# Performance work log

Hardware: AMD Instinct MI355X
Metric: run time of the kernel (lower is better)

Reference implementation:

```python
import jax, jax.numpy as jnp
import numpy as np

B, T = 64, 2048
DQ, A, E = 1024, 128, 512
NF, K = 32, 31
PAD = (K - 1) // 2


def setup_inputs() -> dict:
    key = jax.random.key(0)
    ks = jax.random.split(key, 8)
    s = 0.02
    return {
        "query": jax.random.normal(ks[0], (B, 1, DQ), jnp.float32),
        "memory": jax.random.normal(ks[1], (B, T, E), jnp.float32),
        "attention_weights_cat": jax.random.uniform(ks[2], (B, 2, T), jnp.float32),
        "W_query": jax.random.normal(ks[3], (A, DQ), jnp.float32) * s,
        "W_memory": jax.random.normal(ks[4], (A, E), jnp.float32) * s,
        "conv_w": jax.random.normal(ks[5], (NF, 2, K), jnp.float32) * s,
        "W_loc": jax.random.normal(ks[6], (A, NF), jnp.float32) * s,
        "v": jax.random.normal(ks[7], (1, A), jnp.float32) * s,
    }


def reference(query, memory, attention_weights_cat, W_query, W_memory, conv_w, W_loc, v):
    # projected key: [B, T, A]
    key = jnp.einsum("bte,ae->bta", memory, W_memory)
    # projected query: [B, 1, A]
    q = jnp.einsum("bsd,ad->bsa", query, W_query)
    # location features: Conv1d (2 -> NF, same padding, no bias) then linear to A
    loc = jax.lax.conv_general_dilated(
        attention_weights_cat, conv_w,
        window_strides=(1,), padding=[(PAD, PAD)],
        dimension_numbers=("NCH", "OIH", "NCH"))  # [B, NF, T]
    loc = jnp.einsum("bft,af->bta", loc, W_loc)  # [B, T, A]
    # additive energies -> scalar score per position
    energies = jnp.einsum("bta,oa->bto", jnp.tanh(q + key + loc), v)[..., 0]  # [B, T]
    attention_weights = jax.nn.softmax(energies, axis=1)  # [B, T]
    attention_context = jnp.einsum("bt,bte->be", attention_weights, memory)  # [B, E]
    return attention_context, attention_weights
```

## Files before the change

kernel.cpp:

```cpp
#include <hip/hip_runtime.h>
#include <hip/hip_bf16.h>
#include <stdint.h>

#define B_   64
#define T_   2048
#define DQ_  1024
#define A_   128
#define E_   512
#define NF_  32
#define KW_  31
#define PAD_ 15
#define M_   (B_*T_)
#define KE_  544

typedef __attribute__((ext_vector_type(8))) short bf16x8;
typedef __attribute__((ext_vector_type(4))) float f32x4;

#define OFF_WCAT 0
#define OFF_Q    139264
#define OFF_EN   172032
#define OFF_CF   696320

__device__ inline ushort f2bf(float f) {
  uint32_t u = __float_as_uint(f);
  u += 0x7fffu + ((u >> 16) & 1u);
  return (ushort)(u >> 16);
}
__device__ inline uint32_t pkbf(float a, float b) {
  uint32_t x = __float_as_uint(a), y = __float_as_uint(b);
  x += 0x7fffu + ((x >> 16) & 1u);
  y += 0x7fffu + ((y >> 16) & 1u);
  return (x >> 16) | (y & 0xffff0000u);
}
__device__ inline float tanh_fast(float x) {
  float cx = fminf(fmaxf(x, -15.f), 15.f);
  float e = __expf(2.f * cx);
  return (e - 1.f) / (e + 1.f);
}

__global__ void prep_wcat(const float* __restrict__ wmem, const float* __restrict__ wloc,
                          ushort* __restrict__ wcat) {
  int a = blockIdx.x, tid = threadIdx.x;
  for (int c = tid; c < E_; c += 256) wcat[a*KE_ + c] = f2bf(wmem[a*E_ + c]);
  if (tid < NF_) wcat[a*KE_ + E_ + tid] = f2bf(wloc[a*NF_ + tid]);
}

__global__ void prep_q(const float* __restrict__ query, const float* __restrict__ wq,
                       float* __restrict__ q) {
  __shared__ float qS[DQ_];
  int b = blockIdx.x, tid = threadIdx.x;
  for (int d = tid; d < DQ_; d += 128) qS[d] = query[b*DQ_ + d];
  __syncthreads();
  const float* wr = wq + (long)tid*DQ_;
  float s = 0.f;
  for (int d = 0; d < DQ_; d += 4) {
    float4 w4 = *(const float4*)(wr + d);
    s = fmaf(qS[d],   w4.x, s); s = fmaf(qS[d+1], w4.y, s);
    s = fmaf(qS[d+2], w4.z, s); s = fmaf(qS[d+3], w4.w, s);
  }
  q[b*A_ + tid] = s;
}

__global__ void conv_kernel(const float* __restrict__ aw, const float* __restrict__ cw,
                            float* __restrict__ convf) {
  __shared__ float awS[2][288];
  __shared__ float cwS[NF_*2*KW_];
  int bid = blockIdx.x;
  int b = bid >> 3, tc = bid & 7, t0 = tc*256;
  int tid = threadIdx.x;
  for (int i = tid; i < 286; i += 256) {
    int g = t0 + i - PAD_;
    bool ok = (g >= 0) && (g < T_);
    awS[0][i] = ok ? aw[(long)b*2*T_ + g]       : 0.f;
    awS[1][i] = ok ? aw[(long)b*2*T_ + T_ + g]  : 0.f;
  }
  for (int i = tid; i < NF_*2*KW_; i += 256) cwS[i] = cw[i];
  __syncthreads();
  float* outp = convf + ((long)(b*T_ + t0 + tid))*NF_;
  #pragma unroll 1
  for (int f = 0; f < NF_; ++f) {
    const float* c0 = &cwS[f*2*KW_];
    float s = 0.f;
    #pragma unroll
    for (int k = 0; k < KW_; ++k) {
      s = fmaf(awS[0][tid + k], c0[k],       s);
      s = fmaf(awS[1][tid + k], c0[KW_ + k], s);
    }
    outp[f] = s;
  }
}

__launch_bounds__(256)
__global__ void energy_kernel(const float* __restrict__ memf, const float* __restrict__ convf,
                              const ushort* __restrict__ wcat, const float* __restrict__ q,
                              const float* __restrict__ vvec, float* __restrict__ energies) {
  __shared__ uint4 As4[1024];
  __shared__ uint4 Bs4[1024];
  __shared__ float epS[256];
  const int tid  = threadIdx.x;
  const int lane = tid & 63, wid = tid >> 6;
  const int wm = wid >> 1, wn = wid & 1;
  const int fr = lane & 15, fk = lane >> 4;
  const long row0 = (long)blockIdx.x * 128;
  const int b = (int)(row0 >> 11);

  f32x4 acc[4][4];
  #pragma unroll
  for (int m = 0; m < 4; ++m)
    #pragma unroll
    for (int n = 0; n < 4; ++n) acc[m][n] = (f32x4){0.f,0.f,0.f,0.f};

  for (int kt = 0; kt < 9; ++kt) {
    __syncthreads();
    if (kt < 8) {
      const int k0 = kt*64;
      #pragma unroll
      for (int i = 0; i < 4; ++i) {
        int c = i*256 + tid;
        int r = c >> 3, cl = c & 7;
        const float* src = memf + (row0 + r)*E_ + k0 + cl*8;
        float4 x = *(const float4*)src;
        float4 y = *(const float4*)(src + 4);
        uint4 p = { pkbf(x.x,x.y), pkbf(x.z,x.w), pkbf(y.x,y.y), pkbf(y.z,y.w) };
        As4[r*8 + (cl ^ (r & 7))] = p;
      }
      #pragma unroll
      for (int i = 0; i < 4; ++i) {
        int c = i*256 + tid;
        int r = c >> 3, cd = c & 7;
        int cl = cd ^ (r & 7);
        const ushort* src = wcat + r*KE_ + k0 + cl*8;
        __builtin_amdgcn_global_load_lds((const __attribute__((address_space(1))) void*)src,
                                         (__attribute__((address_space(3))) void*)(Bs4 + c),
                                         16, 0, 0);
      }
    } else {
      #pragma unroll
      for (int i = 0; i < 2; ++i) {
        int c = i*256 + tid;
        int r = c >> 2, cl = c & 3;
        const float* src = convf + (row0 + r)*NF_ + cl*8;
        float4 x = *(const float4*)src;
        float4 y = *(const float4*)(src + 4);
        uint4 p = { pkbf(x.x,x.y), pkbf(x.z,x.w), pkbf(y.x,y.y), pkbf(y.z,y.w) };
        As4[r*8 + (cl ^ (r & 7))] = p;
      }
      #pragma unroll
      for (int i = 0; i < 2; ++i) {
        int c = i*256 + tid;
        int r = c >> 2, cl = c & 3;
        uint4 w = *(const uint4*)(wcat + r*KE_ + E_ + cl*8);
        Bs4[r*8 + (cl ^ (r & 7))] = w;
      }
    }
    __syncthreads();
    const ushort* As = (const ushort*)As4;
    const ushort* Bs = (const ushort*)Bs4;
    const int nkk = (kt < 8) ? 2 : 1;
    for (int kk = 0; kk < nkk; ++kk) {
      bf16x8 af[4], bfr[4];
      const int clk = kk*4 + fk;
      #pragma unroll
      for (int m = 0; m < 4; ++m) {
        int r = wm*64 + m*16 + fr;
        af[m] = *(const bf16x8*)(As + r*64 + (clk ^ (r & 7))*8);
      }
      #pragma unroll
      for (int n = 0; n < 4; ++n) {
        int r = wn*64 + n*16 + fr;
        bfr[n] = *(const bf16x8*)(Bs + r*64 + (clk ^ (r & 7))*8);
      }
      #pragma unroll
      for (int m = 0; m < 4; ++m)
        #pragma unroll
        for (int n = 0; n < 4; ++n)
          acc[m][n] = __builtin_amdgcn_mfma_f32_16x16x32_bf16(af[m], bfr[n], acc[m][n], 0, 0, 0);
    }
  }

  const float* qb = q + b*A_;
  float ep[4][4];
  #pragma unroll
  for (int m = 0; m < 4; ++m)
    #pragma unroll
    for (int r = 0; r < 4; ++r) ep[m][r] = 0.f;
  #pragma unroll
  for (int n = 0; n < 4; ++n) {
    int col = wn*64 + n*16 + fr;
    float qa = qb[col];
    float va = vvec[col];
    #pragma unroll
    for (int m = 0; m < 4; ++m)
      #pragma unroll
      for (int r = 0; r < 4; ++r)
        ep[m][r] = fmaf(va, tanh_fast(acc[m][n][r] + qa), ep[m][r]);
  }
  #pragma unroll
  for (int m = 0; m < 4; ++m)
    #pragma unroll
    for (int r = 0; r < 4; ++r) {
      float v = ep[m][r];
      v += __shfl_xor(v, 1); v += __shfl_xor(v, 2);
      v += __shfl_xor(v, 4); v += __shfl_xor(v, 8);
      ep[m][r] = v;
    }
  if (fr == 0) {
    #pragma unroll
    for (int m = 0; m < 4; ++m)
      #pragma unroll
      for (int r = 0; r < 4; ++r)
        epS[wn*128 + wm*64 + m*16 + fk*4 + r] = ep[m][r];
  }
  __syncthreads();
  if (tid < 128) energies[row0 + tid] = epS[tid] + epS[128 + tid];
}

__global__ void softmax_kernel(const float* __restrict__ energies, float* __restrict__ outw) {
  __shared__ float redm[4], reds[4];
  int b = blockIdx.x, tid = threadIdx.x;
  int lane = tid & 63, wid = tid >> 6;
  const float* e = energies + (long)b*T_;
  float v[8];
  float m = -1e30f;
  #pragma unroll
  for (int i = 0; i < 8; ++i) { v[i] = e[tid + i*256]; m = fmaxf(m, v[i]); }
  #pragma unroll
  for (int o = 32; o > 0; o >>= 1) m = fmaxf(m, __shfl_xor(m, o));
  if (lane == 0) redm[wid] = m;
  __syncthreads();
  m = fmaxf(fmaxf(redm[0], redm[1]), fmaxf(redm[2], redm[3]));
  float s = 0.f;
  #pragma unroll
  for (int i = 0; i < 8; ++i) { v[i] = __expf(v[i] - m); s += v[i]; }
  #pragma unroll
  for (int o = 32; o > 0; o >>= 1) s += __shfl_xor(s, o);
  if (lane == 0) reds[wid] = s;
  __syncthreads();
  s = reds[0] + reds[1] + reds[2] + reds[3];
  float inv = 1.f / s;
  #pragma unroll
  for (int i = 0; i < 8; ++i) outw[(long)b*T_ + tid + i*256] = v[i] * inv;
}

__global__ void context_kernel(const float* __restrict__ memf, const float* __restrict__ w,
                               float* __restrict__ ctx) {
  int bid = blockIdx.x;
  int b = bid >> 3, tc = bid & 7;
  int tid = threadIdx.x;
  const float* wrow  = w + (long)b*T_ + tc*256;
  const float* mbase = memf + ((long)b*T_ + tc*256)*E_;
  float a0 = 0.f, a1 = 0.f;
  #pragma unroll 4
  for (int t = 0; t < 256; ++t) {
    float wt = wrow[t];
    const float* mr = mbase + (long)t*E_;
    a0 = fmaf(wt, mr[tid],       a0);
    a1 = fmaf(wt, mr[tid + 256], a1);
  }
  atomicAdd(&ctx[b*E_ + tid],       a0);
  atomicAdd(&ctx[b*E_ + tid + 256], a1);
}

extern "C" void kernel_launch(void* const* d_in, const int* in_sizes, int n_in,
                              void* d_out, int out_size, void* d_ws, size_t ws_size,
                              hipStream_t stream) {
  const float* query  = (const float*)d_in[0];
  const float* memory = (const float*)d_in[1];
  const float* awcat  = (const float*)d_in[2];
  const float* wq     = (const float*)d_in[3];
  const float* wmem   = (const float*)d_in[4];
  const float* convw  = (const float*)d_in[5];
  const float* wloc   = (const float*)d_in[6];
  const float* vvec   = (const float*)d_in[7];

  char* ws = (char*)d_ws;
  ushort* wcat    = (ushort*)(ws + OFF_WCAT);
  float*  qproj   = (float*)(ws + OFF_Q);
  float*  energies= (float*)(ws + OFF_EN);
  float*  convf   = (float*)(ws + OFF_CF);

  float* ctx  = (float*)d_out;
  float* outw = (float*)d_out + B_*E_;

  hipMemsetAsync(ctx, 0, B_*E_*sizeof(float), stream);
  prep_wcat<<<128, 256, 0, stream>>>(wmem, wloc, wcat);
  prep_q<<<64, 128, 0, stream>>>(query, wq, qproj);
  conv_kernel<<<512, 256, 0, stream>>>(awcat, convw, convf);
  energy_kernel<<<1024, 256, 0, stream>>>(memory, convf, wcat, qproj, vvec, energies);
  softmax_kernel<<<64, 256, 0, stream>>>(energies, outw);
  context_kernel<<<512, 256, 0, stream>>>(memory, outw, ctx);
}
```

Before: 544.8 us.

## Fuse conv into energy GEMM and merge softmax with context via block stats

Computes the location convolution in the energy kernel's final K-step straight from shared memory, so the separate conv kernel and its convf round trip through global memory are gone. The energy kernel also emits a per-block max and exp-sum. A new kernel then combines those stats into the global softmax, writes the weights, and accumulates context over 128-row chunks with 1024 blocks instead of 512. This saves two launches and memory traffic. In exchange, the conv work is redundant across the A/B tiles, and the extra shared memory may lower energy-kernel occupancy.

New measurement: 534.9 us. Within noise of the previous version (-1.8%).

```diff
diff --git a/kernel.cpp b/kernel.cpp
--- a/kernel.cpp
+++ b/kernel.cpp
@@ -10,7 +10,6 @@
 #define NF_  32
 #define KW_  31
 #define PAD_ 15
-#define M_   (B_*T_)
 #define KE_  544
 
 typedef __attribute__((ext_vector_type(8))) short bf16x8;
@@ -19,7 +18,7 @@
 #define OFF_WCAT 0
 #define OFF_Q    139264
 #define OFF_EN   172032
-#define OFF_CF   696320
+#define OFF_ST   696320
 
 __device__ inline ushort f2bf(float f) {
   uint32_t u = __float_as_uint(f);
@@ -61,48 +60,32 @@
   q[b*A_ + tid] = s;
 }
 
-__global__ void conv_kernel(const float* __restrict__ aw, const float* __restrict__ cw,
-                            float* __restrict__ convf) {
-  __shared__ float awS[2][288];
-  __shared__ float cwS[NF_*2*KW_];
-  int bid = blockIdx.x;
-  int b = bid >> 3, tc = bid & 7, t0 = tc*256;
-  int tid = threadIdx.x;
-  for (int i = tid; i < 286; i += 256) {
-    int g = t0 + i - PAD_;
-    bool ok = (g >= 0) && (g < T_);
-    awS[0][i] = ok ? aw[(long)b*2*T_ + g]       : 0.f;
-    awS[1][i] = ok ? aw[(long)b*2*T_ + T_ + g]  : 0.f;
-  }
-  for (int i = tid; i < NF_*2*KW_; i += 256) cwS[i] = cw[i];
-  __syncthreads();
-  float* outp = convf + ((long)(b*T_ + t0 + tid))*NF_;
-  #pragma unroll 1
-  for (int f = 0; f < NF_; ++f) {
-    const float* c0 = &cwS[f*2*KW_];
-    float s = 0.f;
-    #pragma unroll
-    for (int k = 0; k < KW_; ++k) {
-      s = fmaf(awS[0][tid + k], c0[k],       s);
-      s = fmaf(awS[1][tid + k], c0[KW_ + k], s);
-    }
-    outp[f] = s;
-  }
-}
-
 __launch_bounds__(256)
-__global__ void energy_kernel(const float* __restrict__ memf, const float* __restrict__ convf,
-                              const ushort* __restrict__ wcat, const float* __restrict__ q,
-                              const float* __restrict__ vvec, float* __restrict__ energies) {
+__global__ void energy_kernel(const float* __restrict__ memf, const float* __restrict__ aw,
+                              const float* __restrict__ cw, const ushort* __restrict__ wcat,
+                              const float* __restrict__ q, const float* __restrict__ vvec,
+                              float* __restrict__ energies, float* __restrict__ stats) {
   __shared__ uint4 As4[1024];
   __shared__ uint4 Bs4[1024];
   __shared__ float epS[256];
+  __shared__ float awS[2][160];
+  __shared__ float cwS[NF_*2*KW_];
+  __shared__ float redS[4];
   const int tid  = threadIdx.x;
   const int lane = tid & 63, wid = tid >> 6;
   const int wm = wid >> 1, wn = wid & 1;
   const int fr = lane & 15, fk = lane >> 4;
   const long row0 = (long)blockIdx.x * 128;
   const int b = (int)(row0 >> 11);
+  const int t0 = (int)(row0 & (T_-1));
+
+  for (int i = tid; i < 158; i += 256) {
+    int g = t0 + i - PAD_;
+    bool ok = (g >= 0) && (g < T_);
+    awS[0][i] = ok ? aw[(long)b*2*T_ + g]      : 0.f;
+    awS[1][i] = ok ? aw[(long)b*2*T_ + T_ + g] : 0.f;
+  }
+  for (int i = tid; i < NF_*2*KW_; i += 256) cwS[i] = cw[i];
 
   f32x4 acc[4][4];
   #pragma unroll
@@ -139,10 +122,19 @@
       for (int i = 0; i < 2; ++i) {
         int c = i*256 + tid;
         int r = c >> 2, cl = c & 3;
-        const float* src = convf + (row0 + r)*NF_ + cl*8;
-        float4 x = *(const float4*)src;
-        float4 y = *(const float4*)(src + 4);
-        uint4 p = { pkbf(x.x,x.y), pkbf(x.z,x.w), pkbf(y.x,y.y), pkbf(y.z,y.w) };
+        float f[8];
+        #pragma unroll
+        for (int j = 0; j < 8; ++j) {
+          const float* c0 = &cwS[(cl*8 + j)*2*KW_];
+          float s = 0.f;
+          #pragma unroll
+          for (int k = 0; k < KW_; ++k) {
+            s = fmaf(awS[0][r + k], c0[k],       s);
+            s = fmaf(awS[1][r + k], c0[KW_ + k], s);
+          }
+          f[j] = s;
+        }
+        uint4 p = { pkbf(f[0],f[1]), pkbf(f[2],f[3]), pkbf(f[4],f[5]), pkbf(f[6],f[7]) };
         As4[r*8 + (cl ^ (r & 7))] = p;
       }
       #pragma unroll
@@ -212,53 +204,62 @@
         epS[wn*128 + wm*64 + m*16 + fk*4 + r] = ep[m][r];
   }
   __syncthreads();
-  if (tid < 128) energies[row0 + tid] = epS[tid] + epS[128 + tid];
-}
-
-__global__ void softmax_kernel(const float* __restrict__ energies, float* __restrict__ outw) {
-  __shared__ float redm[4], reds[4];
-  int b = blockIdx.x, tid = threadIdx.x;
-  int lane = tid & 63, wid = tid >> 6;
-  const float* e = energies + (long)b*T_;
-  float v[8];
-  float m = -1e30f;
-  #pragma unroll
-  for (int i = 0; i < 8; ++i) { v[i] = e[tid + i*256]; m = fmaxf(m, v[i]); }
-  #pragma unroll
-  for (int o = 32; o > 0; o >>= 1) m = fmaxf(m, __shfl_xor(m, o));
-  if (lane == 0) redm[wid] = m;
-  __syncthreads();
-  m = fmaxf(fmaxf(redm[0], redm[1]), fmaxf(redm[2], redm[3]));
-  float s = 0.f;
-  #pragma unroll
-  for (int i = 0; i < 8; ++i) { v[i] = __expf(v[i] - m); s += v[i]; }
-  #pragma unroll
-  for (int o = 32; o > 0; o >>= 1) s += __shfl_xor(s, o);
-  if (lane == 0) reds[wid] = s;
-  __syncthreads();
-  s = reds[0] + reds[1] + reds[2] + reds[3];
-  float inv = 1.f / s;
-  #pragma unroll
-  for (int i = 0; i < 8; ++i) outw[(long)b*T_ + tid + i*256] = v[i] * inv;
-}
-
-__global__ void context_kernel(const float* __restrict__ memf, const float* __restrict__ w,
-                               float* __restrict__ ctx) {
-  int bid = blockIdx.x;
-  int b = bid >> 3, tc = bid & 7;
-  int tid = threadIdx.x;
-  const float* wrow  = w + (long)b*T_ + tc*256;
-  const float* mbase = memf + ((long)b*T_ + tc*256)*E_;
-  float a0 = 0.f, a1 = 0.f;
-  #pragma unroll 4
-  for (int t = 0; t < 256; ++t) {
-    float wt = wrow[t];
-    const float* mr = mbase + (long)t*E_;
-    a0 = fmaf(wt, mr[tid],       a0);
-    a1 = fmaf(wt, mr[tid + 256], a1);
-  }
-  atomicAdd(&ctx[b*E_ + tid],       a0);
-  atomicAdd(&ctx[b*E_ + tid + 256], a1);
+  float e = -1e30f;
+  if (tid < 128) {
+    e = epS[tid] + epS[128 + tid];
+    energies[row0 + tid] = e;
+  }
+  float mx = e;
+  #pragma unroll
+  for (int o = 32; o > 0; o >>= 1) mx = fmaxf(mx, __shfl_xor(mx, o));
+  if (lane == 0) redS[wid] = mx;
+  __syncthreads();
+  mx = fmaxf(fmaxf(redS[0], redS[1]), fmaxf(redS[2], redS[3]));
+  float sx = (tid < 128) ? __expf(e - mx) : 0.f;
+  #pragma unroll
+  for (int o = 32; o > 0; o >>= 1) sx += __shfl_xor(sx, o);
+  __syncthreads();
+  if (lane == 0) redS[wid] = sx;
+  __syncthreads();
+  if (tid == 0) {
+    stats[2*blockIdx.x]     = mx;
+    stats[2*blockIdx.x + 1] = redS[0] + redS[1] + redS[2] + redS[3];
+  }
+}
+
+__launch_bounds__(256)
+__global__ void smctx_kernel(const float* __restrict__ memf, const float* __restrict__ energies,
+                             const float* __restrict__ stats, float* __restrict__ outw,
+                             float* __restrict__ ctx) {
+  __shared__ float wS[128];
+  const int blk = blockIdx.x;
+  const int b = blk >> 4;
+  const int t0 = (blk & 15) * 128;
+  const int tid = threadIdx.x;
+  float M = -1e30f;
+  #pragma unroll
+  for (int j = 0; j < 16; ++j) M = fmaxf(M, stats[2*(b*16 + j)]);
+  float Z = 0.f;
+  #pragma unroll
+  for (int j = 0; j < 16; ++j) Z += stats[2*(b*16 + j) + 1] * __expf(stats[2*(b*16 + j)] - M);
+  const float invZ = 1.f / Z;
+  if (tid < 128) {
+    float w = __expf(energies[(long)b*T_ + t0 + tid] - M) * invZ;
+    outw[(long)b*T_ + t0 + tid] = w;
+    wS[tid] = w;
+  }
+  __syncthreads();
+  const float* mb = memf + ((long)b*T_ + t0)*E_;
+  float ax = 0.f, ay = 0.f;
+  #pragma unroll 8
+  for (int t = 0; t < 128; ++t) {
+    float wt = wS[t];
+    float2 m2 = *(const float2*)(mb + (long)t*E_ + tid*2);
+    ax = fmaf(wt, m2.x, ax);
+    ay = fmaf(wt, m2.y, ay);
+  }
+  atomicAdd(&ctx[b*E_ + tid*2],     ax);
+  atomicAdd(&ctx[b*E_ + tid*2 + 1], ay);
 }
 
 extern "C" void kernel_launch(void* const* d_in, const int* in_sizes, int n_in,
@@ -277,7 +278,7 @@
   ushort* wcat    = (ushort*)(ws + OFF_WCAT);
   float*  qproj   = (float*)(ws + OFF_Q);
   float*  energies= (float*)(ws + OFF_EN);
-  float*  convf   = (float*)(ws + OFF_CF);
+  float*  stats   = (float*)(ws + OFF_ST);
 
   float* ctx  = (float*)d_out;
   float* outw = (float*)d_out + B_*E_;
@@ -285,8 +286,7 @@
   hipMemsetAsync(ctx, 0, B_*E_*sizeof(float), stream);
   prep_wcat<<<128, 256, 0, stream>>>(wmem, wloc, wcat);
   prep_q<<<64, 128, 0, stream>>>(query, wq, qproj);
-  conv_kernel<<<512, 256, 0, stream>>>(awcat, convw, convf);
-  energy_kernel<<<1024, 256, 0, stream>>>(memory, convf, wcat, qproj, vvec, energies);
-  softmax_kernel<<<64, 256, 0, stream>>>(energies, outw);
-  context_kernel<<<512, 256, 0, stream>>>(memory, outw, ctx);
-}
+  energy_kernel<<<1024, 256, 0, stream>>>(memory, awcat, convw, wcat, qproj, vvec,
+                                          energies, stats);
+  smctx_kernel<<<1024, 256, 0, stream>>>(memory, energies, stats, outw, ctx);
+}
```
